# Performance work log

Hardware: AMD Instinct MI355X
Metric: run time of the kernel (lower is better)

The kernel has to match this reference:

```python
import jax, jax.numpy as jnp
import numpy as np

N_NODES = 50000
N_EDGES = 600000
D = 128


def _mlp(x, Wa, ba, Wb, bb):
    # 2-layer MLP: Linear -> ReLU -> Linear
    h = jax.nn.relu(x @ Wa + ba)
    return h @ Wb + bb


def _gin_layer(h, src, dst, Wa, ba, Wb, bb):
    # GINConv (sum aggregator, eps=0): apply_func(h + sum_{j in N(i)} h_j)
    agg = jax.ops.segment_sum(h[src], dst, num_segments=N_NODES)
    return _mlp(h + agg, Wa, ba, Wb, bb)


def setup_inputs() -> dict:
    key = jax.random.key(0)
    ks = jax.random.split(key, 8)
    s = 1.0 / np.sqrt(D)
    return {
        "inputs": jax.random.normal(ks[0], (N_NODES, D), dtype=jnp.float32),
        "src": jax.random.randint(ks[1], (N_EDGES,), 0, N_NODES, dtype=jnp.int32),
        "dst": jax.random.randint(ks[2], (N_EDGES,), 0, N_NODES, dtype=jnp.int32),
        "W1a": jax.random.normal(ks[3], (D, D), dtype=jnp.float32) * s,
        "b1a": jnp.zeros((D,), dtype=jnp.float32),
        "W1b": jax.random.normal(ks[4], (D, D), dtype=jnp.float32) * s,
        "b1b": jnp.zeros((D,), dtype=jnp.float32),
        "W2a": jax.random.normal(ks[5], (D, D), dtype=jnp.float32) * s,
        "b2a": jnp.zeros((D,), dtype=jnp.float32),
        "W2b": jax.random.normal(ks[6], (D, D), dtype=jnp.float32) * s,
        "b2b": jnp.zeros((D,), dtype=jnp.float32),
    }


def reference(inputs, src, dst, W1a, b1a, W1b, b1b, W2a, b2a, W2b, b2b):
    h = _gin_layer(inputs, src, dst, W1a, b1a, W1b, b1b)
    h = jax.nn.relu(h)
    h = _gin_layer(h, src, dst, W2a, b2a, W2b, b2b)
    return h
```

## Files before the change

kernel.cpp:

```cpp
#include <hip/hip_runtime.h>
#include <hip/hip_bf16.h>
#include <stdint.h>

#define N_NODES 50000
#define N_EDGES 600000
#define D 128
#define BM 16
#define NBLK (N_NODES / BM)
#define CAP 64
#define DUMMY N_NODES

typedef __attribute__((ext_vector_type(8))) short bf16x8_t;
typedef __attribute__((ext_vector_type(4))) float f32x4;

__device__ __forceinline__ float bf2f(ushort u) {
    union { uint32_t u; float f; } v;
    v.u = ((uint32_t)u) << 16;
    return v.f;
}
__device__ __forceinline__ ushort f2bf(float f) {
    union { float f; uint32_t u; } v; v.f = f;
    uint32_t u = v.u;
    return (ushort)((u + 0x7fffu + ((u >> 16) & 1u)) >> 16);
}


__global__ __launch_bounds__(256) void init_kernel(int* __restrict__ cur,
                                                   ushort* __restrict__ ibuf,
                                                   ushort* __restrict__ hbuf) {
    int i = blockIdx.x * 256 + threadIdx.x;
    if (i < N_NODES) cur[i] = i << 6;
    if (i < D) {
        ibuf[(size_t)DUMMY * D + i] = 0;
        hbuf[(size_t)DUMMY * D + i] = 0;
    }
}


__global__ __launch_bounds__(256) void scatter_prep(const int* __restrict__ src,
                                                    const int* __restrict__ dst,
                                                    int* __restrict__ cur,
                                                    int* __restrict__ csr,
                                                    const float* __restrict__ in,
                                                    ushort* __restrict__ ibuf,
                                                    const float* __restrict__ W1a,
                                                    const float* __restrict__ W1b,
                                                    const float* __restrict__ W2a,
                                                    const float* __restrict__ W2b,
                                                    ushort* __restrict__ wbuf) {
    int tid = blockIdx.x * 256 + threadIdx.x;
    int stride = gridDim.x * 256;
    for (int e = tid; e < N_EDGES; e += stride) {
        int d = dst[e];
        int slot = atomicAdd(&cur[d], 1);
        csr[slot] = src[e];
    }
    const int total4 = N_NODES * 32;
    for (int i = tid; i < total4; i += stride) {
        float4 v = ((const float4*)in)[i];
        ushort4 o;
        o.x = f2bf(v.x); o.y = f2bf(v.y); o.z = f2bf(v.z); o.w = f2bf(v.w);
        ((ushort4*)ibuf)[i] = o;
    }
    for (int idx = tid; idx < 65536; idx += stride) {
        const float* srcs[4] = {W1a, W1b, W2a, W2b};
        int mat = idx >> 14;
        int n = (idx >> 7) & 127;
        int k = idx & 127;
        wbuf[idx] = f2bf(srcs[mat][k * 128 + n]);
    }
}


template <int OUT_BF16>
__global__ __launch_bounds__(256) void gin_layer(const ushort* __restrict__ h,
                                                 const int* __restrict__ cur,
                                                 const int* __restrict__ csr,
                                                 const ushort* __restrict__ Wat,
                                                 const float* __restrict__ ba,
                                                 const ushort* __restrict__ Wbt,
                                                 const float* __restrict__ bb,
                                                 void* __restrict__ outp) {
    __shared__ ushort xs[BM][136];
    __shared__ ushort hs[BM][136];
    int tid = threadIdx.x;
    int row0 = blockIdx.x * BM;

    {
        int r = tid >> 4;
        int q = tid & 15;
        int row = row0 + r;
        const ushort* hq = h + q * 8;
        float acc[8];
        {
            bf16x8_t t0 = *(const bf16x8_t*)(hq + (size_t)row * D);
            #pragma unroll
            for (int j = 0; j < 8; ++j) acc[j] = bf2f((ushort)t0[j]);
        }
        int sbase = row << 6;
        int n = cur[row] - sbase;
        const int4* cp = (const int4*)(csr + sbase);
        int full = n >> 2;
        int rem = n & 3;
        int4 ii = cp[0];
        for (int it = 0; it < full; ++it) {
            int4 ci = ii;
            ii = (it + 1 < full) ? cp[it + 1] : ii;
            bf16x8_t a0 = *(const bf16x8_t*)(hq + (size_t)ci.x * D);
            bf16x8_t a1 = *(const bf16x8_t*)(hq + (size_t)ci.y * D);
            bf16x8_t a2 = *(const bf16x8_t*)(hq + (size_t)ci.z * D);
            bf16x8_t a3 = *(const bf16x8_t*)(hq + (size_t)ci.w * D);
            #pragma unroll
            for (int j = 0; j < 8; ++j) {
                acc[j] += (bf2f((ushort)a0[j]) + bf2f((ushort)a1[j]))
                        + (bf2f((ushort)a2[j]) + bf2f((ushort)a3[j]));
            }
        }
        {
            int4 ci = cp[full];
            int i0 = (rem > 0) ? ci.x : DUMMY;
            int i1 = (rem > 1) ? ci.y : DUMMY;
            int i2 = (rem > 2) ? ci.z : DUMMY;
            bf16x8_t a0 = *(const bf16x8_t*)(hq + (size_t)i0 * D);
            bf16x8_t a1 = *(const bf16x8_t*)(hq + (size_t)i1 * D);
            bf16x8_t a2 = *(const bf16x8_t*)(hq + (size_t)i2 * D);
            #pragma unroll
            for (int j = 0; j < 8; ++j) {
                acc[j] += bf2f((ushort)a0[j]) + bf2f((ushort)a1[j])
                        + bf2f((ushort)a2[j]);
            }
        }
        bf16x8_t o0;
        #pragma unroll
        for (int j = 0; j < 8; ++j) o0[j] = (short)f2bf(acc[j]);
        *(bf16x8_t*)&xs[r][q * 8] = o0;
    }
    __syncthreads();

    int w = tid >> 6;
    int l = tid & 63;
    int lr = l & 15;
    int g = l >> 4;
    int ch = w * 32;

    {
        bf16x8_t a[4];
        #pragma unroll
        for (int c = 0; c < 4; ++c)
            a[c] = *(const bf16x8_t*)&xs[lr][32 * c + 8 * g];

        #pragma unroll
        for (int nt = 0; nt < 2; ++nt) {
            int col = ch + 16 * nt + lr;
            f32x4 c4 = {0.f, 0.f, 0.f, 0.f};
            const ushort* wrow = Wat + (size_t)col * D + g * 8;
            #pragma unroll
            for (int c = 0; c < 4; ++c) {
                bf16x8_t b = *(const bf16x8_t*)(wrow + 32 * c);
                c4 = __builtin_amdgcn_mfma_f32_16x16x32_bf16(a[c], b, c4, 0, 0, 0);
            }
            float bv = ba[col];
            #pragma unroll
            for (int r = 0; r < 4; ++r) {
                float v = fmaxf(c4[r] + bv, 0.f);
                hs[g * 4 + r][col] = f2bf(v);
            }
        }
    }
    __syncthreads();

    {
        bf16x8_t a2[4];
        #pragma unroll
        for (int c = 0; c < 4; ++c)
            a2[c] = *(const bf16x8_t*)&hs[lr][32 * c + 8 * g];

        #pragma unroll
        for (int nt = 0; nt < 2; ++nt) {
            int col = ch + 16 * nt + lr;
            f32x4 c4 = {0.f, 0.f, 0.f, 0.f};
            const ushort* wrow = Wbt + (size_t)col * D + g * 8;
            #pragma unroll
            for (int c = 0; c < 4; ++c) {
                bf16x8_t b = *(const bf16x8_t*)(wrow + 32 * c);
                c4 = __builtin_amdgcn_mfma_f32_16x16x32_bf16(a2[c], b, c4, 0, 0, 0);
            }
            float bv = bb[col];
            #pragma unroll
            for (int r = 0; r < 4; ++r) {
                int row = row0 + g * 4 + r;
                float v = c4[r] + bv;
                if (OUT_BF16)
                    ((ushort*)outp)[(size_t)row * D + col] = f2bf(fmaxf(v, 0.f));
                else
                    ((float*)outp)[(size_t)row * D + col] = v;
            }
        }
    }
}


extern "C" void kernel_launch(void* const* d_in, const int* in_sizes, int n_in,
                              void* d_out, int out_size, void* d_ws, size_t ws_size,
                              hipStream_t stream) {
    const float* inputs = (const float*)d_in[0];
    const int* src = (const int*)d_in[1];
    const int* dst = (const int*)d_in[2];
    const float* W1a = (const float*)d_in[3];
    const float* b1a = (const float*)d_in[4];
    const float* W1b = (const float*)d_in[5];
    const float* b1b = (const float*)d_in[6];
    const float* W2a = (const float*)d_in[7];
    const float* b2a = (const float*)d_in[8];
    const float* W2b = (const float*)d_in[9];
    const float* b2b = (const float*)d_in[10];
    float* out = (float*)d_out;

    int* cur = (int*)d_ws;
    int* csr = cur + N_NODES;
    ushort* wbuf = (ushort*)(((uintptr_t)(csr + (size_t)N_NODES * CAP + 16) + 255)
                             & ~(uintptr_t)255);
    ushort* W1at = wbuf;
    ushort* W1bt = wbuf + 16384;
    ushort* W2at = wbuf + 2 * 16384;
    ushort* W2bt = wbuf + 3 * 16384;
    ushort* ibuf = wbuf + 4 * 16384;
    ushort* hbuf = ibuf + (size_t)(N_NODES + 1) * D;

    init_kernel<<<(N_NODES + 255) / 256, 256, 0, stream>>>(cur, ibuf, hbuf);
    scatter_prep<<<2048, 256, 0, stream>>>(src, dst, cur, csr, inputs, ibuf,
                                           W1a, W1b, W2a, W2b, wbuf);

    gin_layer<1><<<NBLK, 256, 0, stream>>>(ibuf, cur, csr,
                                           W1at, b1a, W1bt, b1b, (void*)hbuf);
    gin_layer<0><<<NBLK, 256, 0, stream>>>(hbuf, cur, csr,
                                           W2at, b2a, W2bt, b2b, (void*)out);
}
```

Measured before the change: 150.0 us.

## Use 16-bit CSR indices, gather eight neighbours per step, stage bf16 output

Neighbour indices are stored as 16-bit values instead of 32-bit, which halves index traffic and lets one 16-byte load fetch eight neighbour ids. The aggregation loop now issues eight row gathers per iteration instead of four, so more loads are in flight. The remainder step always issues eight loads, with unused slots pointing at the zero dummy row. The first layer's bf16 output is staged through shared memory and written as coalesced 16-byte rows rather than scattered 2-byte stores. The 16-bit indices only work because the node count (50000) and the dummy index fit below 65536, so this breaks for larger graphs.

```diff
diff --git a/kernel.cpp b/kernel.cpp
--- a/kernel.cpp
+++ b/kernel.cpp
@@ -11,6 +11,7 @@
 #define DUMMY N_NODES
 
 typedef __attribute__((ext_vector_type(8))) short bf16x8_t;
+typedef __attribute__((ext_vector_type(8))) ushort ushort8_t;
 typedef __attribute__((ext_vector_type(4))) float f32x4;
 
 __device__ __forceinline__ float bf2f(ushort u) {
@@ -40,7 +41,7 @@
 __global__ __launch_bounds__(256) void scatter_prep(const int* __restrict__ src,
                                                     const int* __restrict__ dst,
                                                     int* __restrict__ cur,
-                                                    int* __restrict__ csr,
+                                                    ushort* __restrict__ csr,
                                                     const float* __restrict__ in,
                                                     ushort* __restrict__ ibuf,
                                                     const float* __restrict__ W1a,
@@ -53,7 +54,7 @@
     for (int e = tid; e < N_EDGES; e += stride) {
         int d = dst[e];
         int slot = atomicAdd(&cur[d], 1);
-        csr[slot] = src[e];
+        csr[slot] = (ushort)src[e];
     }
     const int total4 = N_NODES * 32;
     for (int i = tid; i < total4; i += stride) {
@@ -75,7 +76,7 @@
 template <int OUT_BF16>
 __global__ __launch_bounds__(256) void gin_layer(const ushort* __restrict__ h,
                                                  const int* __restrict__ cur,
-                                                 const int* __restrict__ csr,
+                                                 const ushort* __restrict__ csr,
                                                  const ushort* __restrict__ Wat,
                                                  const float* __restrict__ ba,
                                                  const ushort* __restrict__ Wbt,
@@ -99,35 +100,49 @@
         }
         int sbase = row << 6;
         int n = cur[row] - sbase;
-        const int4* cp = (const int4*)(csr + sbase);
-        int full = n >> 2;
-        int rem = n & 3;
-        int4 ii = cp[0];
+        const ushort* cp = csr + sbase;
+        int full = n >> 3;
+        int rem = n & 7;
+        ushort8_t ii = *(const ushort8_t*)cp;
         for (int it = 0; it < full; ++it) {
-            int4 ci = ii;
-            ii = (it + 1 < full) ? cp[it + 1] : ii;
-            bf16x8_t a0 = *(const bf16x8_t*)(hq + (size_t)ci.x * D);
-            bf16x8_t a1 = *(const bf16x8_t*)(hq + (size_t)ci.y * D);
-            bf16x8_t a2 = *(const bf16x8_t*)(hq + (size_t)ci.z * D);
-            bf16x8_t a3 = *(const bf16x8_t*)(hq + (size_t)ci.w * D);
+            ushort8_t ci = ii;
+            int nx = (it + 1 < full) ? (it + 1) * 8 : it * 8;
+            ii = *(const ushort8_t*)(cp + nx);
+            bf16x8_t g0 = *(const bf16x8_t*)(hq + (size_t)ci[0] * D);
+            bf16x8_t g1 = *(const bf16x8_t*)(hq + (size_t)ci[1] * D);
+            bf16x8_t g2 = *(const bf16x8_t*)(hq + (size_t)ci[2] * D);
+            bf16x8_t g3 = *(const bf16x8_t*)(hq + (size_t)ci[3] * D);
+            bf16x8_t g4 = *(const bf16x8_t*)(hq + (size_t)ci[4] * D);
+            bf16x8_t g5 = *(const bf16x8_t*)(hq + (size_t)ci[5] * D);
+            bf16x8_t g6 = *(const bf16x8_t*)(hq + (size_t)ci[6] * D);
+            bf16x8_t g7 = *(const bf16x8_t*)(hq + (size_t)ci[7] * D);
             #pragma unroll
             for (int j = 0; j < 8; ++j) {
-                acc[j] += (bf2f((ushort)a0[j]) + bf2f((ushort)a1[j]))
-                        + (bf2f((ushort)a2[j]) + bf2f((ushort)a3[j]));
+                acc[j] += ((bf2f((ushort)g0[j]) + bf2f((ushort)g1[j]))
+                         + (bf2f((ushort)g2[j]) + bf2f((ushort)g3[j])))
+                        + ((bf2f((ushort)g4[j]) + bf2f((ushort)g5[j]))
+                         + (bf2f((ushort)g6[j]) + bf2f((ushort)g7[j])));
             }
         }
         {
-            int4 ci = cp[full];
-            int i0 = (rem > 0) ? ci.x : DUMMY;
-            int i1 = (rem > 1) ? ci.y : DUMMY;
-            int i2 = (rem > 2) ? ci.z : DUMMY;
-            bf16x8_t a0 = *(const bf16x8_t*)(hq + (size_t)i0 * D);
-            bf16x8_t a1 = *(const bf16x8_t*)(hq + (size_t)i1 * D);
-            bf16x8_t a2 = *(const bf16x8_t*)(hq + (size_t)i2 * D);
+            ushort8_t ci = *(const ushort8_t*)(cp + full * 8);
+            int idx[8];
+            #pragma unroll
+            for (int j = 0; j < 8; ++j) idx[j] = (j < rem) ? (int)ci[j] : DUMMY;
+            bf16x8_t g0 = *(const bf16x8_t*)(hq + (size_t)idx[0] * D);
+            bf16x8_t g1 = *(const bf16x8_t*)(hq + (size_t)idx[1] * D);
+            bf16x8_t g2 = *(const bf16x8_t*)(hq + (size_t)idx[2] * D);
+            bf16x8_t g3 = *(const bf16x8_t*)(hq + (size_t)idx[3] * D);
+            bf16x8_t g4 = *(const bf16x8_t*)(hq + (size_t)idx[4] * D);
+            bf16x8_t g5 = *(const bf16x8_t*)(hq + (size_t)idx[5] * D);
+            bf16x8_t g6 = *(const bf16x8_t*)(hq + (size_t)idx[6] * D);
+            bf16x8_t g7 = *(const bf16x8_t*)(hq + (size_t)idx[7] * D);
             #pragma unroll
             for (int j = 0; j < 8; ++j) {
-                acc[j] += bf2f((ushort)a0[j]) + bf2f((ushort)a1[j])
-                        + bf2f((ushort)a2[j]);
+                acc[j] += ((bf2f((ushort)g0[j]) + bf2f((ushort)g1[j]))
+                         + (bf2f((ushort)g2[j]) + bf2f((ushort)g3[j])))
+                        + ((bf2f((ushort)g4[j]) + bf2f((ushort)g5[j]))
+                         + (bf2f((ushort)g6[j]) + bf2f((ushort)g7[j])));
             }
         }
         bf16x8_t o0;
@@ -190,12 +205,20 @@
             for (int r = 0; r < 4; ++r) {
                 int row = row0 + g * 4 + r;
                 float v = c4[r] + bv;
-                if (OUT_BF16)
-                    ((ushort*)outp)[(size_t)row * D + col] = f2bf(fmaxf(v, 0.f));
-                else
+                if (OUT_BF16) {
+                    xs[g * 4 + r][col] = f2bf(fmaxf(v, 0.f));
+                } else {
                     ((float*)outp)[(size_t)row * D + col] = v;
-            }
-        }
+                }
+            }
+        }
+    }
+    if (OUT_BF16) {
+        __syncthreads();
+        int rr = tid >> 4;
+        int qq = tid & 15;
+        *(bf16x8_t*)((ushort*)outp + (size_t)(row0 + rr) * D + qq * 8) =
+            *(const bf16x8_t*)&xs[rr][qq * 8];
     }
 }
 
@@ -217,8 +240,8 @@
     float* out = (float*)d_out;
 
     int* cur = (int*)d_ws;
-    int* csr = cur + N_NODES;
-    ushort* wbuf = (ushort*)(((uintptr_t)(csr + (size_t)N_NODES * CAP + 16) + 255)
+    ushort* csr = (ushort*)(cur + N_NODES);
+    ushort* wbuf = (ushort*)(((uintptr_t)(csr + (size_t)N_NODES * CAP + 64) + 255)
                              & ~(uintptr_t)255);
     ushort* W1at = wbuf;
     ushort* W1bt = wbuf + 16384;
```

New measurement: 132.9 us. 11.4% less time.
